# Kernel optimization log

Measured on AMD Instinct MI355X. Metric: run time of the kernel, lower is better.

The kernel has to match this reference:

```python
import jax, jax.numpy as jnp
import numpy as np

TOP_K = 32
OBS_RADIUS = 1.0
N = 4096
IN_DIM = 4


def setup_inputs() -> dict:
    key = jax.random.key(0)
    ks = jax.random.split(key, 10)
    s = 0.05
    return {
        "states": jax.random.normal(ks[0], (N, 4), jnp.float32),
        "goals": jax.random.normal(ks[1], (N, 2), jnp.float32),
        "W1": jax.random.normal(ks[2], (64, IN_DIM + 1), jnp.float32) * s,
        "b1": jnp.zeros((64,), jnp.float32),
        "W2": jax.random.normal(ks[3], (128, 64), jnp.float32) * s,
        "b2": jnp.zeros((128,), jnp.float32),
        "Wd1": jax.random.normal(ks[4], (64, 132), jnp.float32) * s,
        "bd1": jnp.zeros((64,), jnp.float32),
        "Wd2": jax.random.normal(ks[5], (128, 64), jnp.float32) * s,
        "bd2": jnp.zeros((128,), jnp.float32),
        "Wd3": jax.random.normal(ks[6], (64, 128), jnp.float32) * s,
        "bd3": jnp.zeros((64,), jnp.float32),
        "Wd4": jax.random.normal(ks[7], (4, 64), jnp.float32) * s,
        "bd4": jnp.zeros((4,), jnp.float32),
    }


def reference(states, goals, W1, b1, W2, b2, Wd1, bd1, Wd2, bd2, Wd3, bd3, Wd4, bd4):
    n = states.shape[0]
    dt = states.dtype
    # pairwise relative states + one-hot self indicator -> [N, N, 5]
    x = states[:, None, :] - states[None, :, :]
    x = jnp.concatenate([x, jnp.eye(n, dtype=dt)[:, :, None]], axis=2)
    # remove_distant_agents: keep TOP_K nearest neighbors by planar distance
    d = jnp.sqrt(jnp.sum(x[:, :, :2] ** 2, axis=2) + 1e-4)  # [N, N]
    _, idx = jax.lax.top_k(-d, TOP_K)                        # [N, K]
    xk = jnp.take_along_axis(x, idx[:, :, None], axis=1)     # [N, K, 5]
    # observation-radius mask (torch reshape [N,K,1]->[N,1,K] == transpose here)
    dist = jnp.linalg.norm(xk[:, :, :2], axis=2)             # [N, K]
    mask = (dist < OBS_RADIUS).astype(dt).reshape(n, 1, TOP_K)
    # NOTE: original uses a raw reshape [N,K,5]->[N,5,K] (not a transpose); match it
    h = xk.reshape(n, IN_DIM + 1, TOP_K)
    # pointwise (kernel-1) conv stack 5 -> 64 -> 128
    h = jax.nn.relu(jnp.einsum('oc,ncp->nop', W1, h) + b1[None, :, None])
    h = jax.nn.relu(jnp.einsum('oc,ncp->nop', W2, h) + b2[None, :, None])
    # original does torch.max(...)[1]: ARGMAX indices, promoted to float by cat
    x_local = jnp.argmax(h * mask, axis=2).astype(dt)        # [N, 128]
    rel = states[:, :2] - goals
    feat = jnp.concatenate([x_local, rel, states[:, 2:]], axis=1)  # [N, 132]
    z = jax.nn.relu(feat @ Wd1.T + bd1)
    z = jax.nn.relu(z @ Wd2.T + bd2)
    z = jax.nn.relu(z @ Wd3.T + bd3)
    z = z @ Wd4.T + bd4
    k = 2.0 * jax.nn.sigmoid(z) + 0.2                        # [N, 4] gains
    state = jnp.concatenate([rel, states[:, 2:]], axis=1)    # [N, 4]
    a_x = -(k[:, 0] * state[:, 0] + k[:, 1] * state[:, 2])
    a_y = -(k[:, 2] * state[:, 1] + k[:, 3] * state[:, 3])
    return jnp.stack([a_x, a_y], axis=1)                     # [N, 2]
```

## Files before the change

kernel.cpp:

```cpp
#include <hip/hip_runtime.h>
#include <math.h>

#define NAGENT 4096
#define TOPK 32
#define FAGB 8
#define CANDCAP 2048

__global__ __launch_bounds__(256) void topk_kernel(
    const float* __restrict__ states, int* __restrict__ idx_out)
{
    const int i = blockIdx.x;
    const int t = threadIdx.x;
    __shared__ unsigned int hist[1024];
    __shared__ unsigned int ps[256];
    __shared__ unsigned int ps2[32];
    __shared__ unsigned long long cand[CANDCAP];
    __shared__ int ccount;
    __shared__ unsigned int cutB;

    #pragma unroll
    for (int u = 0; u < 4; ++u) hist[t + u * 256] = 0u;
    if (t == 0) ccount = 0;

    const float4 si = ((const float4*)states)[i];
    __syncthreads();

    unsigned int mybits[16];
    #pragma unroll
    for (int u = 0; u < 16; ++u) {
        int j = t + u * 256;
        float4 sj = ((const float4*)states)[j];
        float dx = __fsub_rn(si.x, sj.x);
        float dy = __fsub_rn(si.y, sj.y);
        float s  = __fadd_rn(__fadd_rn(__fmul_rn(dx, dx), __fmul_rn(dy, dy)), 1e-4f);
        float dv = sqrtf(s);
        mybits[u] = __float_as_uint(dv);
        unsigned int bin = (unsigned int)(dv * 256.0f);
        if (bin > 1023u) bin = 1023u;
        atomicAdd(&hist[bin], 1u);
    }
    __syncthreads();

    ps[t] = hist[t * 4 + 0] + hist[t * 4 + 1] + hist[t * 4 + 2] + hist[t * 4 + 3];
    __syncthreads();
    if (t < 32) {
        unsigned int s = 0;
        #pragma unroll
        for (int q = 0; q < 8; ++q) s += ps[t * 8 + q];
        ps2[t] = s;
    }
    __syncthreads();

    if (t == 0) {
        unsigned int cum = 0;
        int g2 = 0;
        while (cum + ps2[g2] < TOPK) { cum += ps2[g2]; ++g2; }
        int g1 = g2 * 8;
        while (cum + ps[g1] < TOPK) { cum += ps[g1]; ++g1; }
        int b = g1 * 4;
        for (;;) { cum += hist[b]; if (cum >= TOPK) break; ++b; }
        cutB = (unsigned int)b;
    }
    __syncthreads();

    const unsigned int B = cutB;
    #pragma unroll
    for (int u = 0; u < 16; ++u) {
        float dv = __uint_as_float(mybits[u]);
        unsigned int bin = (unsigned int)(dv * 256.0f);
        if (bin > 1023u) bin = 1023u;
        if (bin <= B) {
            int pos = atomicAdd(&ccount, 1);
            if (pos < CANDCAP)
                cand[pos] = ((unsigned long long)mybits[u] << 32)
                          | (unsigned int)(t + u * 256);
        }
    }
    __syncthreads();

    const int C = (ccount < CANDCAP) ? ccount : CANDCAP;
    for (int q = t; q < C; q += 256) {
        unsigned long long key = cand[q];
        int rank = 0;
        for (int r = 0; r < C; ++r) rank += (cand[r] < key) ? 1 : 0;
        if (rank < TOPK) idx_out[i * TOPK + rank] = (int)(key & 0xffffffffu);
    }
}

__global__ __launch_bounds__(256) void fused_kernel(
    const float* __restrict__ states, const float* __restrict__ goals,
    const float* __restrict__ W1,  const float* __restrict__ b1,
    const float* __restrict__ W2,  const float* __restrict__ b2,
    const float* __restrict__ Wd1, const float* __restrict__ bd1,
    const float* __restrict__ Wd2, const float* __restrict__ bd2,
    const float* __restrict__ Wd3, const float* __restrict__ bd3,
    const float* __restrict__ Wd4, const float* __restrict__ bd4,
    const int* __restrict__ idx_in, float* __restrict__ out)
{
    const int t = threadIdx.x;
    const int a = t >> 6;
    const int l = t & 63;
    const int base = blockIdx.x * FAGB;

    __shared__ __attribute__((aligned(16))) float w2a[64 * 68];
    __shared__ __attribute__((aligned(16))) float w2b[64 * 68];
    __shared__ __attribute__((aligned(16))) float w1s[320];
    __shared__ __attribute__((aligned(16))) float b1s[64];
    __shared__ __attribute__((aligned(16))) float b2s[128];
    __shared__ __attribute__((aligned(16))) float flat[4][160];
    __shared__ __attribute__((aligned(16))) float maskv[4][32];
    __shared__ __attribute__((aligned(16))) float featb[FAGB][132];
    __shared__ __attribute__((aligned(16))) float h1[4][2048];
    float* z1s = &h1[0][0];
    float* z2s = z1s + 512;
    float* z3s = z2s + 1024;
    float* kvs = z3s + 512;

    #pragma unroll
    for (int u = 0; u < 32; ++u) {
        int e = t + u * 256;
        int o = e >> 6, c = e & 63;
        float v = W2[e];
        int dst = c * 68 + ((o >> 3) << 2) + (o & 3);
        if (o & 4) w2b[dst] = v; else w2a[dst] = v;
    }
    for (int e = t; e < 320; e += 256) w1s[e] = W1[e];
    if (t < 64)  b1s[t] = b1[t];
    if (t < 128) b2s[t] = b2[t];
    __syncthreads();

    #pragma unroll
    for (int round = 0; round < 2; ++round) {
        const int g = round * 4 + a;
        const int i = base + g;

        if (l < 32) {
            int j = idx_in[i * TOPK + l];
            float4 sj  = ((const float4*)states)[j];
            float4 siv = ((const float4*)states)[i];
            float d0 = siv.x - sj.x;
            float d1 = siv.y - sj.y;
            float d2 = siv.z - sj.z;
            float d3 = siv.w - sj.w;
            flat[a][l * 5 + 0] = d0;
            flat[a][l * 5 + 1] = d1;
            flat[a][l * 5 + 2] = d2;
            flat[a][l * 5 + 3] = d3;
            flat[a][l * 5 + 4] = (j == i) ? 1.0f : 0.0f;
            float dist = sqrtf(__fadd_rn(__fmul_rn(d0, d0), __fmul_rn(d1, d1)));
            maskv[a][l] = (dist < 1.0f) ? 1.0f : 0.0f;
        } else if (l < 36) {
            int f = l - 32;
            float4 siv = ((const float4*)states)[i];
            float2 gi  = ((const float2*)goals)[i];
            float v = (f == 0) ? (siv.x - gi.x)
                    : (f == 1) ? (siv.y - gi.y)
                    : (f == 2) ? siv.z : siv.w;
            featb[g][128 + f] = v;
        }

        #pragma unroll
        for (int u = 0; u < 32; ++u) {
            int e = u * 64 + l;
            int p = e & 31, o1 = e >> 5;
            float acc = b1s[o1];
            #pragma unroll
            for (int f = 0; f < 5; ++f)
                acc += w1s[o1 * 5 + f] * flat[a][f * 32 + p];
            h1[a][o1 * 32 + p] = fmaxf(acc, 0.0f);
        }

        const int ow = l & 15;
        const int pt = l >> 4;
        float acc[8][8];
        #pragma unroll
        for (int k = 0; k < 8; ++k)
            #pragma unroll
            for (int q = 0; q < 8; ++q) acc[k][q] = 0.0f;

        for (int c = 0; c < 64; ++c) {
            float4 wA = *(const float4*)&w2a[c * 68 + ow * 4];
            float4 wB = *(const float4*)&w2b[c * 68 + ow * 4];
            float4 hA = *(const float4*)&h1[a][c * 32 + pt * 8];
            float4 hB = *(const float4*)&h1[a][c * 32 + pt * 8 + 4];
            float wv[8] = {wA.x, wA.y, wA.z, wA.w, wB.x, wB.y, wB.z, wB.w};
            float hv[8] = {hA.x, hA.y, hA.z, hA.w, hB.x, hB.y, hB.z, hB.w};
            #pragma unroll
            for (int k = 0; k < 8; ++k)
                #pragma unroll
                for (int q = 0; q < 8; ++q)
                    acc[k][q] += wv[k] * hv[q];
        }

        float4 mA = *(const float4*)&maskv[a][pt * 8];
        float4 mB = *(const float4*)&maskv[a][pt * 8 + 4];
        float mv[8] = {mA.x, mA.y, mA.z, mA.w, mB.x, mB.y, mB.z, mB.w};
        #pragma unroll
        for (int k = 0; k < 8; ++k) {
            float bb = b2s[ow * 8 + k];
            unsigned long long best = 0ull;
            #pragma unroll
            for (int q = 0; q < 8; ++q) {
                float val = fmaxf(acc[k][q] + bb, 0.0f) * mv[q];
                unsigned long long key =
                    ((unsigned long long)__float_as_uint(val) << 32)
                    | (unsigned int)(31 - (pt * 8 + q));
                if (key > best) best = key;
            }
            unsigned long long o1 = __shfl_xor(best, 16, 64); if (o1 > best) best = o1;
            unsigned long long o2 = __shfl_xor(best, 32, 64); if (o2 > best) best = o2;
            if (pt == 0) {
                int pbest = 31 - (int)(best & 63ull);
                featb[g][ow * 8 + k] = (float)pbest;
            }
        }
    }
    __syncthreads();

    const int g0 = 2 * a, g1 = 2 * a + 1;

    {
        float bb = bd1[l];
        float a0 = bb, a1 = bb;
        for (int k = 0; k < 33; ++k) {
            float4 wv = *(const float4*)&Wd1[l * 132 + 4 * k];
            float4 f0 = *(const float4*)&featb[g0][4 * k];
            float4 f1 = *(const float4*)&featb[g1][4 * k];
            a0 += wv.x * f0.x; a0 += wv.y * f0.y; a0 += wv.z * f0.z; a0 += wv.w * f0.w;
            a1 += wv.x * f1.x; a1 += wv.y * f1.y; a1 += wv.z * f1.z; a1 += wv.w * f1.w;
        }
        z1s[g0 * 64 + l] = fmaxf(a0, 0.0f);
        z1s[g1 * 64 + l] = fmaxf(a1, 0.0f);
    }

    {
        float accA0 = bd2[l], accA1 = bd2[l];
        float accB0 = bd2[l + 64], accB1 = bd2[l + 64];
        for (int k = 0; k < 16; ++k) {
            float4 wa = *(const float4*)&Wd2[l * 64 + 4 * k];
            float4 wb = *(const float4*)&Wd2[(l + 64) * 64 + 4 * k];
            float4 f0 = *(const float4*)&z1s[g0 * 64 + 4 * k];
            float4 f1 = *(const float4*)&z1s[g1 * 64 + 4 * k];
            accA0 += wa.x * f0.x; accA0 += wa.y * f0.y;
            accA0 += wa.z * f0.z; accA0 += wa.w * f0.w;
            accB0 += wb.x * f0.x; accB0 += wb.y * f0.y;
            accB0 += wb.z * f0.z; accB0 += wb.w * f0.w;
            accA1 += wa.x * f1.x; accA1 += wa.y * f1.y;
            accA1 += wa.z * f1.z; accA1 += wa.w * f1.w;
            accB1 += wb.x * f1.x; accB1 += wb.y * f1.y;
            accB1 += wb.z * f1.z; accB1 += wb.w * f1.w;
        }
        z2s[g0 * 128 + l]      = fmaxf(accA0, 0.0f);
        z2s[g0 * 128 + l + 64] = fmaxf(accB0, 0.0f);
        z2s[g1 * 128 + l]      = fmaxf(accA1, 0.0f);
        z2s[g1 * 128 + l + 64] = fmaxf(accB1, 0.0f);
    }

    {
        float bb = bd3[l];
        float a0 = bb, a1 = bb;
        for (int k = 0; k < 32; ++k) {
            float4 wv = *(const float4*)&Wd3[l * 128 + 4 * k];
            float4 f0 = *(const float4*)&z2s[g0 * 128 + 4 * k];
            float4 f1 = *(const float4*)&z2s[g1 * 128 + 4 * k];
            a0 += wv.x * f0.x; a0 += wv.y * f0.y; a0 += wv.z * f0.z; a0 += wv.w * f0.w;
            a1 += wv.x * f1.x; a1 += wv.y * f1.y; a1 += wv.z * f1.z; a1 += wv.w * f1.w;
        }
        z3s[g0 * 64 + l] = fmaxf(a0, 0.0f);
        z3s[g1 * 64 + l] = fmaxf(a1, 0.0f);
    }

    if (l < 8) {
        int gg = (l >> 2) ? g1 : g0;
        int o = l & 3;
        float acc = bd4[o];
        for (int c = 0; c < 64; ++c) acc += Wd4[o * 64 + c] * z3s[gg * 64 + c];
        kvs[gg * 4 + o] = 2.0f / (1.0f + expf(-acc)) + 0.2f;
    }
    if (l < 4) {
        int gg = (l >> 1) ? g1 : g0;
        int axis = l & 1;
        float ka = kvs[gg * 4 + 2 * axis + 0];
        float kb = kvs[gg * 4 + 2 * axis + 1];
        float rel = featb[gg][128 + axis];
        float vel = featb[gg][130 + axis];
        out[(base + gg) * 2 + axis] = -(ka * rel + kb * vel);
    }
}

extern "C" void kernel_launch(void* const* d_in, const int* in_sizes, int n_in,
                              void* d_out, int out_size, void* d_ws, size_t ws_size,
                              hipStream_t stream)
{
    const float* states = (const float*)d_in[0];
    const float* goals  = (const float*)d_in[1];
    const float* W1  = (const float*)d_in[2];
    const float* b1  = (const float*)d_in[3];
    const float* W2  = (const float*)d_in[4];
    const float* b2  = (const float*)d_in[5];
    const float* Wd1 = (const float*)d_in[6];
    const float* bd1 = (const float*)d_in[7];
    const float* Wd2 = (const float*)d_in[8];
    const float* bd2 = (const float*)d_in[9];
    const float* Wd3 = (const float*)d_in[10];
    const float* bd3 = (const float*)d_in[11];
    const float* Wd4 = (const float*)d_in[12];
    const float* bd4 = (const float*)d_in[13];

    int*   idx = (int*)d_ws;
    float* out = (float*)d_out;

    topk_kernel<<<NAGENT, 256, 0, stream>>>(states, idx);
    fused_kernel<<<NAGENT / FAGB, 256, 0, stream>>>(states, goals, W1, b1, W2, b2,
                                                    Wd1, bd1, Wd2, bd2, Wd3, bd3,
                                                    Wd4, bd4, idx, out);
}
```

Baseline: 141.5 us.

## Process 16 agents per block and parallelize top-k histogram cutoff scan

The MLP kernel now handles 16 agents per block instead of 8, running four conv rounds and computing four agents per wave in the dense layers. This amortizes the shared-memory staging of W2 and the global reads of the dense-layer weights over more agents. The top-k kernel replaces the serial single-thread cumulative search over the histogram with a wave-level shuffle prefix scan, so the cutoff bin is found in parallel. The b2 bias is now read from global memory rather than shared memory. Halving the block count reduces parallelism across CUs, and the extra accumulators raise register pressure.

Measured after the change: 155.3 us. 9.7% more time.

```diff
diff --git a/kernel.cpp b/kernel.cpp
--- a/kernel.cpp
+++ b/kernel.cpp
@@ -3,7 +3,7 @@
 
 #define NAGENT 4096
 #define TOPK 32
-#define FAGB 8
+#define FAGB 16
 #define CANDCAP 2048
 
 __global__ __launch_bounds__(256) void topk_kernel(
@@ -11,9 +11,9 @@
 {
     const int i = blockIdx.x;
     const int t = threadIdx.x;
+    const int lane = t & 63;
     __shared__ unsigned int hist[1024];
-    __shared__ unsigned int ps[256];
-    __shared__ unsigned int ps2[32];
+    __shared__ unsigned int wsum[4];
     __shared__ unsigned long long cand[CANDCAP];
     __shared__ int ccount;
     __shared__ unsigned int cutB;
@@ -41,24 +41,30 @@
     }
     __syncthreads();
 
-    ps[t] = hist[t * 4 + 0] + hist[t * 4 + 1] + hist[t * 4 + 2] + hist[t * 4 + 3];
-    __syncthreads();
-    if (t < 32) {
-        unsigned int s = 0;
-        #pragma unroll
-        for (int q = 0; q < 8; ++q) s += ps[t * 8 + q];
-        ps2[t] = s;
-    }
-    __syncthreads();
-
-    if (t == 0) {
-        unsigned int cum = 0;
-        int g2 = 0;
-        while (cum + ps2[g2] < TOPK) { cum += ps2[g2]; ++g2; }
-        int g1 = g2 * 8;
-        while (cum + ps[g1] < TOPK) { cum += ps[g1]; ++g1; }
-        int b = g1 * 4;
-        for (;;) { cum += hist[b]; if (cum >= TOPK) break; ++b; }
+    unsigned int h0 = hist[t * 4 + 0], h1 = hist[t * 4 + 1];
+    unsigned int h2 = hist[t * 4 + 2], h3 = hist[t * 4 + 3];
+    unsigned int v = h0 + h1 + h2 + h3;
+    unsigned int inc = v;
+    #pragma unroll
+    for (int off = 1; off < 64; off <<= 1) {
+        unsigned int u = __shfl_up(inc, off, 64);
+        if (lane >= off) inc += u;
+    }
+    if (lane == 63) wsum[t >> 6] = inc;
+    __syncthreads();
+    unsigned int woff = 0;
+    for (int w = 0; w < (t >> 6); ++w) woff += wsum[w];
+    unsigned int incl = inc + woff;
+    unsigned int exc  = incl - v;
+    if (exc < TOPK && incl >= TOPK) {
+        unsigned int cum = exc;
+        unsigned int hh[4] = {h0, h1, h2, h3};
+        int b = t * 4 + 3;
+        #pragma unroll
+        for (int q = 0; q < 4; ++q) {
+            cum += hh[q];
+            if (cum >= TOPK) { b = t * 4 + q; break; }
+        }
         cutB = (unsigned int)b;
     }
     __syncthreads();
@@ -106,15 +112,14 @@
     __shared__ __attribute__((aligned(16))) float w2b[64 * 68];
     __shared__ __attribute__((aligned(16))) float w1s[320];
     __shared__ __attribute__((aligned(16))) float b1s[64];
-    __shared__ __attribute__((aligned(16))) float b2s[128];
     __shared__ __attribute__((aligned(16))) float flat[4][160];
     __shared__ __attribute__((aligned(16))) float maskv[4][32];
     __shared__ __attribute__((aligned(16))) float featb[FAGB][132];
     __shared__ __attribute__((aligned(16))) float h1[4][2048];
     float* z1s = &h1[0][0];
-    float* z2s = z1s + 512;
-    float* z3s = z2s + 1024;
-    float* kvs = z3s + 512;
+    float* z2s = z1s + 1024;
+    float* z3s = z2s + 2048;
+    float* kvs = z3s + 1024;
 
     #pragma unroll
     for (int u = 0; u < 32; ++u) {
@@ -125,12 +130,11 @@
         if (o & 4) w2b[dst] = v; else w2a[dst] = v;
     }
     for (int e = t; e < 320; e += 256) w1s[e] = W1[e];
-    if (t < 64)  b1s[t] = b1[t];
-    if (t < 128) b2s[t] = b2[t];
-    __syncthreads();
-
-    #pragma unroll
-    for (int round = 0; round < 2; ++round) {
+    if (t < 64) b1s[t] = b1[t];
+    __syncthreads();
+
+    #pragma unroll
+    for (int round = 0; round < 4; ++round) {
         const int g = round * 4 + a;
         const int i = base + g;
 
@@ -197,7 +201,7 @@
         float mv[8] = {mA.x, mA.y, mA.z, mA.w, mB.x, mB.y, mB.z, mB.w};
         #pragma unroll
         for (int k = 0; k < 8; ++k) {
-            float bb = b2s[ow * 8 + k];
+            float bb = b2[ow * 8 + k];
             unsigned long long best = 0ull;
             #pragma unroll
             for (int q = 0; q < 8; ++q) {
@@ -217,74 +221,84 @@
     }
     __syncthreads();
 
-    const int g0 = 2 * a, g1 = 2 * a + 1;
+    const int gbase = a * 4;
 
     {
         float bb = bd1[l];
-        float a0 = bb, a1 = bb;
+        float a0 = bb, a1 = bb, a2 = bb, a3 = bb;
         for (int k = 0; k < 33; ++k) {
             float4 wv = *(const float4*)&Wd1[l * 132 + 4 * k];
-            float4 f0 = *(const float4*)&featb[g0][4 * k];
-            float4 f1 = *(const float4*)&featb[g1][4 * k];
+            float4 f0 = *(const float4*)&featb[gbase + 0][4 * k];
+            float4 f1 = *(const float4*)&featb[gbase + 1][4 * k];
+            float4 f2 = *(const float4*)&featb[gbase + 2][4 * k];
+            float4 f3 = *(const float4*)&featb[gbase + 3][4 * k];
             a0 += wv.x * f0.x; a0 += wv.y * f0.y; a0 += wv.z * f0.z; a0 += wv.w * f0.w;
             a1 += wv.x * f1.x; a1 += wv.y * f1.y; a1 += wv.z * f1.z; a1 += wv.w * f1.w;
-        }
-        z1s[g0 * 64 + l] = fmaxf(a0, 0.0f);
-        z1s[g1 * 64 + l] = fmaxf(a1, 0.0f);
+            a2 += wv.x * f2.x; a2 += wv.y * f2.y; a2 += wv.z * f2.z; a2 += wv.w * f2.w;
+            a3 += wv.x * f3.x; a3 += wv.y * f3.y; a3 += wv.z * f3.z; a3 += wv.w * f3.w;
+        }
+        z1s[(gbase + 0) * 64 + l] = fmaxf(a0, 0.0f);
+        z1s[(gbase + 1) * 64 + l] = fmaxf(a1, 0.0f);
+        z1s[(gbase + 2) * 64 + l] = fmaxf(a2, 0.0f);
+        z1s[(gbase + 3) * 64 + l] = fmaxf(a3, 0.0f);
     }
 
     {
-        float accA0 = bd2[l], accA1 = bd2[l];
-        float accB0 = bd2[l + 64], accB1 = bd2[l + 64];
+        float accA[4], accB[4];
+        float bA = bd2[l], bB = bd2[l + 64];
+        #pragma unroll
+        for (int g = 0; g < 4; ++g) { accA[g] = bA; accB[g] = bB; }
         for (int k = 0; k < 16; ++k) {
             float4 wa = *(const float4*)&Wd2[l * 64 + 4 * k];
             float4 wb = *(const float4*)&Wd2[(l + 64) * 64 + 4 * k];
-            float4 f0 = *(const float4*)&z1s[g0 * 64 + 4 * k];
-            float4 f1 = *(const float4*)&z1s[g1 * 64 + 4 * k];
-            accA0 += wa.x * f0.x; accA0 += wa.y * f0.y;
-            accA0 += wa.z * f0.z; accA0 += wa.w * f0.w;
-            accB0 += wb.x * f0.x; accB0 += wb.y * f0.y;
-            accB0 += wb.z * f0.z; accB0 += wb.w * f0.w;
-            accA1 += wa.x * f1.x; accA1 += wa.y * f1.y;
-            accA1 += wa.z * f1.z; accA1 += wa.w * f1.w;
-            accB1 += wb.x * f1.x; accB1 += wb.y * f1.y;
-            accB1 += wb.z * f1.z; accB1 += wb.w * f1.w;
-        }
-        z2s[g0 * 128 + l]      = fmaxf(accA0, 0.0f);
-        z2s[g0 * 128 + l + 64] = fmaxf(accB0, 0.0f);
-        z2s[g1 * 128 + l]      = fmaxf(accA1, 0.0f);
-        z2s[g1 * 128 + l + 64] = fmaxf(accB1, 0.0f);
+            #pragma unroll
+            for (int g = 0; g < 4; ++g) {
+                float4 f = *(const float4*)&z1s[(gbase + g) * 64 + 4 * k];
+                accA[g] += wa.x * f.x; accA[g] += wa.y * f.y;
+                accA[g] += wa.z * f.z; accA[g] += wa.w * f.w;
+                accB[g] += wb.x * f.x; accB[g] += wb.y * f.y;
+                accB[g] += wb.z * f.z; accB[g] += wb.w * f.w;
+            }
+        }
+        #pragma unroll
+        for (int g = 0; g < 4; ++g) {
+            z2s[(gbase + g) * 128 + l]      = fmaxf(accA[g], 0.0f);
+            z2s[(gbase + g) * 128 + l + 64] = fmaxf(accB[g], 0.0f);
+        }
     }
 
     {
+        float acc[4];
         float bb = bd3[l];
-        float a0 = bb, a1 = bb;
+        #pragma unroll
+        for (int g = 0; g < 4; ++g) acc[g] = bb;
         for (int k = 0; k < 32; ++k) {
             float4 wv = *(const float4*)&Wd3[l * 128 + 4 * k];
-            float4 f0 = *(const float4*)&z2s[g0 * 128 + 4 * k];
-            float4 f1 = *(const float4*)&z2s[g1 * 128 + 4 * k];
-            a0 += wv.x * f0.x; a0 += wv.y * f0.y; a0 += wv.z * f0.z; a0 += wv.w * f0.w;
-            a1 += wv.x * f1.x; a1 += wv.y * f1.y; a1 += wv.z * f1.z; a1 += wv.w * f1.w;
-        }
-        z3s[g0 * 64 + l] = fmaxf(a0, 0.0f);
-        z3s[g1 * 64 + l] = fmaxf(a1, 0.0f);
-    }
-
+            #pragma unroll
+            for (int g = 0; g < 4; ++g) {
+                float4 f = *(const float4*)&z2s[(gbase + g) * 128 + 4 * k];
+                acc[g] += wv.x * f.x; acc[g] += wv.y * f.y;
+                acc[g] += wv.z * f.z; acc[g] += wv.w * f.w;
+            }
+        }
+        #pragma unroll
+        for (int g = 0; g < 4; ++g)
+            z3s[(gbase + g) * 64 + l] = fmaxf(acc[g], 0.0f);
+    }
+
+    if (l < 16) {
+        int g = gbase + (l >> 2), o = l & 3;
+        float acc = bd4[o];
+        for (int c = 0; c < 64; ++c) acc += Wd4[o * 64 + c] * z3s[g * 64 + c];
+        kvs[g * 4 + o] = 2.0f / (1.0f + expf(-acc)) + 0.2f;
+    }
     if (l < 8) {
-        int gg = (l >> 2) ? g1 : g0;
-        int o = l & 3;
-        float acc = bd4[o];
-        for (int c = 0; c < 64; ++c) acc += Wd4[o * 64 + c] * z3s[gg * 64 + c];
-        kvs[gg * 4 + o] = 2.0f / (1.0f + expf(-acc)) + 0.2f;
-    }
-    if (l < 4) {
-        int gg = (l >> 1) ? g1 : g0;
-        int axis = l & 1;
-        float ka = kvs[gg * 4 + 2 * axis + 0];
-        float kb = kvs[gg * 4 + 2 * axis + 1];
-        float rel = featb[gg][128 + axis];
-        float vel = featb[gg][130 + axis];
-        out[(base + gg) * 2 + axis] = -(ka * rel + kb * vel);
+        int g = gbase + (l >> 1), axis = l & 1;
+        float ka = kvs[g * 4 + 2 * axis + 0];
+        float kb = kvs[g * 4 + 2 * axis + 1];
+        float rel = featb[g][128 + axis];
+        float vel = featb[g][130 + axis];
+        out[(base + g) * 2 + axis] = -(ka * rel + kb * vel);
     }
 }
 
```
